# Optimization experiments

Measured on AMD Instinct MI355X. Metric: run time of the kernel, lower is better.

Reference implementation:

```python
import jax, jax.numpy as jnp
import numpy as np
from jax import lax

BATCH, FS, DIM = 32, 7, 512
E, TOPK, KD = 4, 2, 4            # experts, top-k, scan directions
N_STATE, DT_RANK = 16, 32
CAP_FACTOR, EPS, AUX_W = 1.25, 1e-6, 0.01


def _layernorm(x, g, b, eps=1e-5):
    mu = x.mean(-1, keepdims=True)
    var = ((x - mu) ** 2).mean(-1, keepdims=True)
    return (x - mu) * lax.rsqrt(var + eps) * g + b


def setup_inputs() -> dict:
    key = jax.random.key(0)
    ks = jax.random.split(key, 10)
    s = 0.02
    d = DIM
    return {
        "x": jax.random.normal(ks[0], (BATCH, FS, FS, d), jnp.float32),
        "w_gate": jax.random.normal(ks[1], (d, E)) * s,
        "b_gate": jnp.zeros((E,), jnp.float32),
        "in_proj_w": jax.random.normal(ks[2], (E, d, 2 * d)) * s,
        "in_proj_b": jnp.zeros((E, 2 * d), jnp.float32),
        "conv_w": jax.random.normal(ks[3], (E, d, 3, 3)) * s,
        "conv_b": jnp.zeros((E, d), jnp.float32),
        "x_proj_w": jax.random.normal(ks[4], (E, KD, DT_RANK + 2 * N_STATE, d)) * s,
        "dt_proj_w": jax.random.normal(ks[5], (E, KD, d, DT_RANK)) * s,
        "dt_proj_b": jax.random.normal(ks[6], (E, KD, d)) * 0.1,
        "A_log": jnp.log(jax.random.uniform(ks[7], (E, KD, d, N_STATE), minval=1.0, maxval=16.0)),
        "Ds": jnp.ones((E, KD, d), jnp.float32),
        "out_norm_g": jnp.ones((E, d), jnp.float32),
        "out_norm_b": jnp.zeros((E, d), jnp.float32),
        "norm_g": jnp.ones((E, d), jnp.float32),
        "norm_b": jnp.zeros((E, d), jnp.float32),
    }


def _ss2d_expert(x, in_w, in_b, cw, cb, xpw, dtw, dtb, A_log, Ds, og, ob, ng, nb):
    # x: [B,H,W,d]; one SS2D expert (VMamba-style, use_out_proj=False, out_norm=True)
    B, H, W, d = x.shape
    L = H * W
    xz = x @ in_w + in_b                      # [B,H,W,2d]
    xin, z = jnp.split(xz, 2, axis=-1)
    xc = jnp.transpose(xin, (0, 3, 1, 2))     # [B,d,H,W]
    xc = lax.conv_general_dilated(xc, cw[:, None, :, :], (1, 1), 'SAME',
                                  feature_group_count=d,
                                  dimension_numbers=('NCHW', 'OIHW', 'NCHW'))
    xc = jax.nn.silu(xc + cb[None, :, None, None])
    xh = xc.reshape(B, d, L)                              # row-major (h)
    xv = jnp.transpose(xc, (0, 1, 3, 2)).reshape(B, d, L)  # col-major (v)
    xs = jnp.stack([xh, xh[..., ::-1], xv, xv[..., ::-1]], axis=1)  # [B,K,d,L]

    x_dbl = jnp.einsum('bkdl,kcd->bkcl', xs, xpw)
    dt, Bm, Cm = jnp.split(x_dbl, [DT_RANK, DT_RANK + N_STATE], axis=2)
    dt = jnp.einsum('bkrl,kdr->bkdl', dt, dtw) + dtb[None, :, :, None]
    dt = jax.nn.softplus(dt)                  # [B,K,d,L]
    A = -jnp.exp(A_log)                       # [K,d,N]

    def step(h, inp):
        dt_t, B_t, C_t, x_t = inp             # [B,K,d],[B,K,N],[B,K,N],[B,K,d]
        h = h * jnp.exp(dt_t[..., None] * A) + (dt_t * x_t)[..., None] * B_t[:, :, None, :]
        y = jnp.einsum('bkdn,bkn->bkd', h, C_t)
        return h, y

    h0 = jnp.zeros((B, KD, d, N_STATE), x.dtype)
    seq = (jnp.moveaxis(dt, 3, 0), jnp.moveaxis(Bm, 3, 0),
           jnp.moveaxis(Cm, 3, 0), jnp.moveaxis(xs, 3, 0))
    _, ys = lax.scan(step, h0, seq)           # [L,B,K,d]
    ys = jnp.moveaxis(ys, 0, 3) + Ds[None, :, :, None] * xs  # [B,K,d,L]

    y = ys[:, 0] + ys[:, 1, :, ::-1]
    yv = ys[:, 2] + ys[:, 3, :, ::-1]
    y = y + jnp.transpose(yv.reshape(B, d, W, H), (0, 1, 3, 2)).reshape(B, d, L)
    y = jnp.transpose(y.reshape(B, d, H, W), (0, 2, 3, 1))   # [B,H,W,d]
    y = _layernorm(y, og, ob) * jax.nn.silu(z)
    pooled = y.mean(axis=(1, 2))              # adaptive avg pool -> [B,d]
    return _layernorm(pooled, ng, nb)


def reference(x, w_gate, b_gate, in_proj_w, in_proj_b, conv_w, conv_b, x_proj_w,
              dt_proj_w, dt_proj_b, A_log, Ds, out_norm_g, out_norm_b, norm_g, norm_b):
    B = x.shape[0]
    # gate on globally pooled features
    x_flat = x.mean(axis=(1, 2))                              # [B,dim]
    raw = jax.nn.softmax(x_flat @ w_gate + b_gate, axis=-1)   # [B,E]
    capacity = int(CAP_FACTOR * B)
    _, idx = lax.top_k(raw, TOPK)
    mask = jax.nn.one_hot(idx, E, dtype=raw.dtype).sum(axis=1)  # [B,E]
    masked = raw * mask
    denom = masked.sum(0, keepdims=True) + EPS
    gate_scores = masked / denom * capacity
    importance = raw.mean(0)
    load = mask.mean(0)
    aux_loss = AUX_W * jnp.mean((load - importance) ** 2)

    topv, topi = lax.top_k(gate_scores, TOPK)                 # [B,k]
    # dense dispatch: run every expert on the full batch (E small), then gather
    all_out = jax.vmap(_ss2d_expert, in_axes=(None,) + (0,) * 13)(
        x, in_proj_w, in_proj_b, conv_w, conv_b, x_proj_w, dt_proj_w, dt_proj_b,
        A_log, Ds, out_norm_g, out_norm_b, norm_g, norm_b)    # [E,B,dim]
    sel = all_out[topi, jnp.arange(B)[:, None]]               # [B,k,dim]
    mixed = (topv[..., None] * sel).sum(axis=1)               # [B,dim]
    return mixed, aux_loss
```

## Files before the change

kernel.cpp:

```cpp
#include <hip/hip_runtime.h>
#include <hip/hip_bf16.h>

#define B_   32
#define D_   512
#define L_   49
#define E_   4
#define KD_  4
#define NS_  16
#define RK_  32
#define JOBS_ 64

typedef short s16x8 __attribute__((ext_vector_type(8)));
typedef float f32x4v __attribute__((ext_vector_type(4)));
union U4 { uint4 u; s16x8 s; unsigned short us[8]; };

__device__ __forceinline__ float bf2f(unsigned short u){
  union{unsigned int i; float f;} v; v.i = ((unsigned int)u)<<16; return v.f;
}
__device__ __forceinline__ float2 bfp(unsigned int u){
  union{unsigned int i; float f;} a, b; a.i = u<<16; b.i = u & 0xffff0000u;
  return make_float2(a.f, b.f);
}
__device__ __forceinline__ unsigned short f2bfu(float f){
  union{float f; unsigned int i;} u; u.f = f;
  unsigned int r = u.i + 0x7fffu + ((u.i >> 16) & 1u);
  return (unsigned short)(r >> 16);
}
__device__ __forceinline__ float silu_f(float x){ return x / (1.f + expf(-x)); }

__device__ __forceinline__ float fast_exp2(float x){
  return __builtin_amdgcn_exp2f(x);
}
__device__ __forceinline__ float quad_add4(float y){
  float t1 = __uint_as_float(__builtin_amdgcn_mov_dpp(__float_as_uint(y), 0xB1, 0xF, 0xF, true));
  y += t1;
  float t2 = __uint_as_float(__builtin_amdgcn_mov_dpp(__float_as_uint(y), 0x4E, 0xF, 0xF, true));
  y += t2;
  return y;
}
__device__ __forceinline__ unsigned cvtpk_bf16(float lo, float hi){
  unsigned r; asm("v_cvt_pk_bf16_f32 %0, %1, %2" : "=v"(r) : "v"(lo), "v"(hi)); return r;
}

__device__ __forceinline__ int detect_bf(const void* x){
  unsigned short u = ((const unsigned short*)x)[threadIdx.x & 63];
  int e = (u >> 7) & 0xff;
  unsigned long long m = __ballot(e >= 96 && e < 160);
  return __popcll(m) >= 56;
}

__device__ __forceinline__ float ldf(const void* p, size_t i, int bf){
  return bf ? bf2f(((const unsigned short*)p)[i]) : ((const float*)p)[i];
}
struct f8s{ float v[8]; };
__device__ __forceinline__ f8s ldf8(const void* p, size_t i, int bf){
  f8s r;
  if (bf){
    uint4 u = *(const uint4*)((const unsigned short*)p + i);
    float2 x = bfp(u.x), y = bfp(u.y), z = bfp(u.z), w = bfp(u.w);
    r.v[0]=x.x; r.v[1]=x.y; r.v[2]=y.x; r.v[3]=y.y;
    r.v[4]=z.x; r.v[5]=z.y; r.v[6]=w.x; r.v[7]=w.y;
  } else {
    const float4* q = (const float4*)((const float*)p + i);
    float4 a = q[0], b = q[1];
    r.v[0]=a.x; r.v[1]=a.y; r.v[2]=a.z; r.v[3]=a.w;
    r.v[4]=b.x; r.v[5]=b.y; r.v[6]=b.z; r.v[7]=b.w;
  }
  return r;
}
struct f4s{ float v[4]; };
__device__ __forceinline__ f4s ldf4(const void* p, size_t i, int bf){
  f4s r;
  if (bf){
    uint2 u = *(const uint2*)((const unsigned short*)p + i);
    float2 a = bfp(u.x), b = bfp(u.y);
    r.v[0]=a.x; r.v[1]=a.y; r.v[2]=b.x; r.v[3]=b.y;
  } else {
    float4 a = *(const float4*)((const float*)p + i);
    r.v[0]=a.x; r.v[1]=a.y; r.v[2]=a.z; r.v[3]=a.w;
  }
  return r;
}
__device__ __forceinline__ U4 ldbf8(const void* p, size_t i, int bf){
  U4 r;
  if (bf){
    r.u = *(const uint4*)((const unsigned short*)p + i);
  } else {
    const float* q = (const float*)p + i;
    float4 a = *(const float4*)q, b = *(const float4*)(q+4);
    r.u.x = (unsigned)f2bfu(a.x) | ((unsigned)f2bfu(a.y) << 16);
    r.u.y = (unsigned)f2bfu(a.z) | ((unsigned)f2bfu(a.w) << 16);
    r.u.z = (unsigned)f2bfu(b.x) | ((unsigned)f2bfu(b.y) << 16);
    r.u.w = (unsigned)f2bfu(b.z) | ((unsigned)f2bfu(b.w) << 16);
  }
  return r;
}
__device__ __forceinline__ void split8(const float av[8], U4& hi, U4& lo){
  #pragma unroll
  for (int j = 0; j < 8; j++){
    union{float f; unsigned int i;} u; u.f = av[j];
    unsigned short h = (unsigned short)(u.i >> 16);
    hi.us[j] = h;
    lo.us[j] = f2bfu(av[j] - bf2f(h));
  }
}

__device__ __forceinline__ int dirmap(int k, int l){
  if (k == 0) return l;
  if (k == 1) return 48 - l;
  if (k == 2) return (l % 7) * 7 + l / 7;
  int l2 = 48 - l; return (l2 % 7) * 7 + l2 / 7;
}

__global__ __launch_bounds__(256) void k_prep(const void* __restrict__ x,
                                              const void* __restrict__ w,
                                              const void* __restrict__ wg,
                                              const void* __restrict__ bg,
                                              unsigned short* __restrict__ wt,
                                              unsigned short* __restrict__ xbf,
                                              float* __restrict__ logits){
  __shared__ unsigned short tile[64][72];
  __shared__ float red[4][4];
  __shared__ float pool[4][512];
  int bf = detect_bf(x);
  int blk = blockIdx.x;
  int t = threadIdx.x;
  if (blk < 512){
    int e = blk >> 7, cb = (blk >> 3) & 15, db = blk & 7;
    #pragma unroll
    for (int r = 0; r < 4; r++){
      int d  = r*16 + (t>>4);
      int c0 = (t&15)*4;
      size_t g = ((size_t)e*512 + db*64 + d)*1024 + cb*64 + c0;
      if (bf){
        uint2 u = *(const uint2*)((const unsigned short*)w + g);
        tile[c0+0][d] = (unsigned short)(u.x & 0xffffu);
        tile[c0+1][d] = (unsigned short)(u.x >> 16);
        tile[c0+2][d] = (unsigned short)(u.y & 0xffffu);
        tile[c0+3][d] = (unsigned short)(u.y >> 16);
      } else {
        float4 v = *(const float4*)((const float*)w + g);
        tile[c0+0][d] = f2bfu(v.x);
        tile[c0+1][d] = f2bfu(v.y);
        tile[c0+2][d] = f2bfu(v.z);
        tile[c0+3][d] = f2bfu(v.w);
      }
    }
    __syncthreads();
    #pragma unroll
    for (int r = 0; r < 2; r++){
      int o = r*256 + t;
      int c = o >> 3, d0 = (o & 7)*8;
      uint4 v = *(const uint4*)&tile[c][d0];
      *(uint4*)(wt + ((size_t)e*1024 + cb*64 + c)*512 + db*64 + d0) = v;
    }
  } else {
    int b = blk - 512;
    int wave = t >> 6, lane = t & 63;
    int d0 = lane * 8;
    float s8[8] = {};
    for (int l = wave; l < L_; l += 4){
      size_t ix = ((size_t)(b*L_ + l))*D_ + d0;
      U4 xb;
      if (bf){
        xb.u = *(const uint4*)((const unsigned short*)x + ix);
        float2 a = bfp(xb.u.x), bq = bfp(xb.u.y), c = bfp(xb.u.z), dq = bfp(xb.u.w);
        s8[0] += a.x;  s8[1] += a.y;  s8[2] += bq.x; s8[3] += bq.y;
        s8[4] += c.x;  s8[5] += c.y;  s8[6] += dq.x; s8[7] += dq.y;
      } else {
        const float* q = (const float*)x + ix;
        float4 f0 = *(const float4*)q, f1 = *(const float4*)(q+4);
        float av[8] = {f0.x,f0.y,f0.z,f0.w, f1.x,f1.y,f1.z,f1.w};
        #pragma unroll
        for (int j = 0; j < 8; j++){ xb.us[j] = f2bfu(av[j]); s8[j] += av[j]; }
      }
      *(uint4*)(xbf + ix) = xb.u;
    }
    #pragma unroll
    for (int j = 0; j < 8; j++) pool[wave][d0+j] = s8[j];
    __syncthreads();
    float p[4] = {0.f, 0.f, 0.f, 0.f};
    #pragma unroll
    for (int rep = 0; rep < 2; rep++){
      int d = t + rep*256;
      float s = pool[0][d] + pool[1][d] + pool[2][d] + pool[3][d];
      float xfd = s * (1.f/49.f);
      #pragma unroll
      for (int e = 0; e < 4; e++) p[e] = fmaf(xfd, ldf(wg, (size_t)d*E_ + e, bf), p[e]);
    }
    #pragma unroll
    for (int off = 32; off > 0; off >>= 1){
      #pragma unroll
      for (int e = 0; e < 4; e++) p[e] += __shfl_down(p[e], off, 64);
    }
    if (lane == 0){
      #pragma unroll
      for (int e = 0; e < 4; e++) red[wave][e] = p[e];
    }
    __syncthreads();
    if (t < 4)
      logits[b*4 + t] = red[0][t]+red[1][t]+red[2][t]+red[3][t] + ldf(bg, t, bf);
  }
}

__global__ __launch_bounds__(128) void k_gate2(const void* __restrict__ x,
                                               const float* __restrict__ logits,
                                               int* __restrict__ topi, float* __restrict__ topv,
                                               void* __restrict__ out){
  __shared__ float raw[B_*E_];
  __shared__ int   sel[B_];
  __shared__ float den[E_], auxp[E_];
  int bf = detect_bf(x);
  int t = threadIdx.x;
  if (t < B_){
    float l0=logits[t*4+0], l1=logits[t*4+1], l2=logits[t*4+2], l3=logits[t*4+3];
    float m = fmaxf(fmaxf(l0,l1), fmaxf(l2,l3));
    float e0=expf(l0-m), e1=expf(l1-m), e2=expf(l2-m), e3=expf(l3-m);
    float s = e0+e1+e2+e3;
    float r[4] = {e0/s, e1/s, e2/s, e3/s};
    int i1 = 0; float v1 = r[0];
    for (int e = 1; e < 4; e++) if (r[e] > v1){ v1 = r[e]; i1 = e; }
    int i2 = -1; float v2 = -1.f;
    for (int e = 0; e < 4; e++){ if (e == i1) continue; if (r[e] > v2){ v2 = r[e]; i2 = e; } }
    if (i1 < 0 || i1 > 3) i1 = 0;
    if (i2 < 0 || i2 > 3) i2 = (i1 + 1) & 3;
    sel[t] = (1<<i1) | (1<<i2);
    for (int e = 0; e < 4; e++) raw[t*4+e] = r[e];
  }
  __syncthreads();
  if (t < E_){
    float dn = 0.f, imp = 0.f, ld = 0.f;
    for (int b = 0; b < B_; b++){
      float r = raw[b*4+t];
      int bit = (sel[b] >> t) & 1;
      if (bit) dn += r;
      imp += r; ld += (float)bit;
    }
    den[t] = dn + 1e-6f;
    imp *= (1.f/B_); ld *= (1.f/B_);
    float df = ld - imp; auxp[t] = df*df;
  }
  __syncthreads();
  if (t == 0){
    float a = 0.01f * 0.25f * (auxp[0]+auxp[1]+auxp[2]+auxp[3]);
    if (bf) ((unsigned short*)out)[16384] = f2bfu(a);
    else    ((float*)out)[16384] = a;
  }
  if (t < B_){
    float gs[4];
    for (int e = 0; e < 4; e++){
      int bit = (sel[t] >> e) & 1;
      gs[e] = bit ? raw[t*4+e] * 40.f / den[e] : 0.f;
    }
    int i1 = 0; float v1 = gs[0];
    for (int e = 1; e < 4; e++) if (gs[e] > v1){ v1 = gs[e]; i1 = e; }
    int i2 = -1; float v2 = -1e30f;
    for (int e = 0; e < 4; e++){ if (e == i1) continue; if (gs[e] > v2){ v2 = gs[e]; i2 = e; } }
    if (i1 < 0 || i1 > 3) i1 = 0;
    if (i2 < 0 || i2 > 3) i2 = (i1 + 1) & 3;
    topi[t*2+0] = i1; topv[t*2+0] = v1;
    topi[t*2+1] = i2; topv[t*2+1] = v2;
  }
}

__global__ __launch_bounds__(256, 4) void k_inproj_mfma(const void* __restrict__ x,
                                                     const unsigned short* __restrict__ xbf,
                                                     const unsigned short* __restrict__ wt,
                                                     const void* __restrict__ bias,
                                                     const void* __restrict__ cw,
                                                     const void* __restrict__ cb,
                                                     const int* __restrict__ topi,
                                                     unsigned short* __restrict__ zbuf,
                                                     float* __restrict__ xc,
                                                     unsigned short* __restrict__ xchi,
                                                     unsigned short* __restrict__ xclo){
  __shared__ float xzt[49*68];
  int bf = detect_bf(x);
  int job = blockIdx.x, nt = blockIdx.y;
  int b = job >> 1;
  int e = topi[job];
  int t = threadIdx.x;
  int wave = t >> 6, lane = t & 63;
  int l16 = lane & 15, quad = lane >> 4;
  int arow = wave*16 + l16; if (arow > 48) arow = 48;
  size_t abase = ((size_t)(b*L_ + arow))*D_;
  int ct = nt*64;
  size_t bbase = ((size_t)(e*1024 + ct + l16))*D_;
  f32x4v acc[4] = {};
  #pragma unroll
  for (int k0 = 0; k0 < 512; k0 += 32){
    int k = k0 + quad*8;
    U4 a; a.u = *(const uint4*)(xbf + abase + k);
    #pragma unroll
    for (int s = 0; s < 4; s++){
      U4 bb;
      bb.u = *(const uint4*)(wt + bbase + (size_t)s*16*D_ + k);
      acc[s] = __builtin_amdgcn_mfma_f32_16x16x32_bf16(a.s, bb.s, acc[s], 0, 0, 0);
    }
  }
  int rb = wave*16 + quad*4;
  if (nt >= 8){
    #pragma unroll
    for (int s = 0; s < 4; s++){
      int c = ct + s*16 + l16;
      float bv = ldf(bias, (size_t)e*1024 + c, bf);
      #pragma unroll
      for (int r = 0; r < 4; r++){
        int row = rb + r;
        if (row < L_)
          zbuf[(size_t)job*25088 + row*D_ + (c - 512)] = f2bfu(acc[s][r] + bv);
      }
    }
    return;
  }
  #pragma unroll
  for (int s = 0; s < 4; s++){
    int cl = s*16 + l16;
    float bv = ldf(bias, (size_t)e*1024 + ct + cl, bf);
    #pragma unroll
    for (int r = 0; r < 4; r++){
      int row = rb + r;
      if (row < L_) xzt[row*68 + cl] = acc[s][r] + bv;
    }
  }
  __syncthreads();
  int c = t & 63, pg = t >> 6;
  int dch = ct + c;
  float wv[9];
  #pragma unroll
  for (int j = 0; j < 9; j++) wv[j] = ldf(cw, ((size_t)(e*D_ + dch))*9 + j, bf);
  float cbv = ldf(cb, (size_t)e*D_ + dch, bf);
  for (int p = pg; p < L_; p += 4){
    int h = p / 7, w = p % 7;
    float a2 = cbv;
    #pragma unroll
    for (int dy = 0; dy < 3; dy++){
      int hh = h + dy - 1; if (hh < 0 || hh >= 7) continue;
      #pragma unroll
      for (int dx = 0; dx < 3; dx++){
        int ww = w + dx - 1; if (ww < 0 || ww >= 7) continue;
        a2 = fmaf(xzt[(hh*7+ww)*68 + c], wv[dy*3+dx], a2);
      }
    }
    float sv = a2 * (1.f/(1.f+expf(-a2)));
    size_t oix = (size_t)job*25088 + (size_t)p*D_ + dch;
    xc[oix] = sv;
    unsigned int ui = __float_as_uint(sv);
    unsigned short hh2 = (unsigned short)(ui >> 16);
    xchi[oix] = hh2;
    xclo[oix] = f2bfu(sv - bf2f(hh2));
  }
}

__global__ __launch_bounds__(256, 4) void k_xproj(const void* __restrict__ x,
                                               const void* __restrict__ xpw,
                                               const int* __restrict__ topi,
                                               const unsigned short* __restrict__ xchi,
                                               const unsigned short* __restrict__ xclo,
                                               float* __restrict__ xdbl){
  int bf = detect_bf(x);
  int kq = blockIdx.x, job = blockIdx.y;
  int k = kq & 3, q = kq >> 2;
  int t = threadIdx.x;
  int wave = t >> 6, lane = t & 63;
  int l16 = lane & 15, quad = lane >> 4;
  int e = topi[job];
  int arow = q*16 + l16; if (arow > 48) arow = 48;
  int m = dirmap(k, arow);
  const unsigned short* ahp = xchi + (size_t)job*25088 + (size_t)m*D_;
  const unsigned short* alp = xclo + (size_t)job*25088 + (size_t)m*D_;
  size_t bbase = (((size_t)(e*KD_+k))*64 + wave*16 + l16)*D_;
  f32x4v acc = {};
  #pragma unroll
  for (int k0 = 0; k0 < 512; k0 += 32){
    int kk = k0 + quad*8;
    U4 Ahi, Alo;
    Ahi.u = *(const uint4*)(ahp + kk);
    Alo.u = *(const uint4*)(alp + kk);
    U4 bb = ldbf8(xpw, bbase + kk, bf);
    acc = __builtin_amdgcn_mfma_f32_16x16x32_bf16(Ahi.s, bb.s, acc, 0, 0, 0);
    acc = __builtin_amdgcn_mfma_f32_16x16x32_bf16(Alo.s, bb.s, acc, 0, 0, 0);
  }
  float* outb = xdbl + ((size_t)(job*KD_+k))*3136;
  int rb = q*16 + quad*4;
  int c = wave*16 + l16;
  #pragma unroll
  for (int r = 0; r < 4; r++){
    int row = rb + r;
    if (row < L_) outb[row*64 + c] = acc[r];
  }
}

__global__ __launch_bounds__(256, 2) void k_scan(const void* __restrict__ x,
                                              const void* __restrict__ dtw,
                                              const void* __restrict__ dtb_,
                                              const void* __restrict__ alog,
                                              const void* __restrict__ ds_,
                                              const int* __restrict__ topi,
                                              const float* __restrict__ xc,
                                              const float* __restrict__ xdbl,
                                              unsigned short* __restrict__ ybuf){
  int bf = detect_bf(x);
  int kz = blockIdx.x, job = blockIdx.y;
  int k = kz & 3, dz2 = kz >> 2;
  int t = threadIdx.x;
  int e = topi[job];
  int ek = e*KD_ + k;
  __shared__ float bc[49*32];
  __shared__ float dtl[49*260];
  const float* xdb = xdbl + ((size_t)(job*KD_+k))*3136;
  {
    const float4* src4 = (const float4*)xdb;
    for (int i = t; i < 392; i += 256){
      int row = i >> 3, c = i & 7;
      ((float4*)bc)[row*8 + c] = src4[row*16 + 8 + c];
    }
  }
  int w = t >> 6, lane = t & 63;
  {
    int l16 = lane & 15, quad4 = lane >> 4;
    U4 Bv[4];
    #pragma unroll
    for (int nt = 0; nt < 4; nt++){
      int d = dz2*256 + w*64 + nt*16 + l16;
      Bv[nt] = ldbf8(dtw, ((size_t)ek*D_ + d)*RK_ + quad4*8, bf);
    }
    f32x4v acc[4][4] = {};
    #pragma unroll
    for (int rt = 0; rt < 4; rt++){
      int arow = rt*16 + l16; if (arow > 48) arow = 48;
      const float* ap = xdb + arow*64 + quad4*8;
      float4 f0 = *(const float4*)ap, f1 = *(const float4*)(ap+4);
      float av[8] = {f0.x,f0.y,f0.z,f0.w, f1.x,f1.y,f1.z,f1.w};
      U4 Ahi, Alo;
      split8(av, Ahi, Alo);
      #pragma unroll
      for (int nt = 0; nt < 4; nt++){
        acc[rt][nt] = __builtin_amdgcn_mfma_f32_16x16x32_bf16(Ahi.s, Bv[nt].s, acc[rt][nt], 0, 0, 0);
        acc[rt][nt] = __builtin_amdgcn_mfma_f32_16x16x32_bf16(Alo.s, Bv[nt].s, acc[rt][nt], 0, 0, 0);
      }
    }
    #pragma unroll
    for (int nt = 0; nt < 4; nt++){
      int d = dz2*256 + w*64 + nt*16 + l16;
      float bias = ldf(dtb_, (size_t)ek*D_ + d, bf);
      int dloc = w*64 + nt*16 + l16;
      #pragma unroll
      for (int rt = 0; rt < 4; rt++){
        #pragma unroll
        for (int r = 0; r < 4; r++){
          int l = rt*16 + quad4*4 + r;
          if (l < L_){
            float v = acc[rt][nt][r] + bias;
            dtl[l*260 + dloc] = fmaxf(v, 0.f) + __logf(1.f + __expf(-fabsf(v)));
          }
        }
      }
    }
  }
  int q4 = (lane >> 2) * 4;
  int ng = lane & 3;
  int dgl = dz2*256 + w*64 + q4;
  float A2[4][4], Dsv[4];
  #pragma unroll
  for (int jj = 0; jj < 4; jj++){
    int dj = dgl + jj;
    f4s ar = ldf4(alog, ((size_t)ek*D_ + dj)*NS_ + ng*4, bf);
    #pragma unroll
    for (int n = 0; n < 4; n++) A2[jj][n] = -expf(ar.v[n]) * 1.44269504f;
    Dsv[jj] = ldf(ds_, (size_t)ek*D_ + dj, bf);
  }
  __syncthreads();
  float h[4][4];
  #pragma unroll
  for (int jj = 0; jj < 4; jj++)
    #pragma unroll
    for (int n = 0; n < 4; n++) h[jj][n] = 0.f;
  const float* xcb = xc + (size_t)job*25088;
  unsigned short* yb = ybuf + ((size_t)(job*KD_ + k))*25088;
  int dtbase = w*64 + q4;
  for (int c0 = 0; c0 < 49; c0 += 7){
    float4 xv[7];
    #pragma unroll
    for (int j = 0; j < 7; j++){
      int m = dirmap(k, c0 + j);
      xv[j] = *(const float4*)(xcb + (size_t)m*D_ + dgl);
    }
    #pragma unroll
    for (int j = 0; j < 7; j++){
      int l = c0 + j;
      float4 dt4 = *(const float4*)&dtl[l*260 + dtbase];
      float4 B4 = *(const float4*)&bc[l*32 + ng*4];
      float4 C4 = *(const float4*)&bc[l*32 + 16 + ng*4];
      float Ba[4] = {B4.x, B4.y, B4.z, B4.w};
      float Ca[4] = {C4.x, C4.y, C4.z, C4.w};
      float dta[4] = {dt4.x, dt4.y, dt4.z, dt4.w};
      float xa[4]  = {xv[j].x, xv[j].y, xv[j].z, xv[j].w};
      float ys[4];
      #pragma unroll
      for (int jj = 0; jj < 4; jj++){
        float dt = dta[jj], x_t = xa[jj];
        float dtx = dt * x_t;
        float y = 0.f;
        #pragma unroll
        for (int n = 0; n < 4; n++){
          float en = fast_exp2(dt * A2[jj][n]);
          h[jj][n] = fmaf(h[jj][n], en, dtx * Ba[n]);
          y = fmaf(h[jj][n], Ca[n], y);
        }
        y = quad_add4(y);
        ys[jj] = fmaf(Dsv[jj], x_t, y);
      }
      if (ng == 0){
        uint2 o;
        o.x = cvtpk_bf16(ys[0], ys[1]);
        o.y = cvtpk_bf16(ys[2], ys[3]);
        *(uint2*)(yb + (size_t)l*D_ + dgl) = o;
      }
    }
  }
}

__global__ __launch_bounds__(512) void k_final_a(const void* __restrict__ x,
                                                 const void* __restrict__ og,
                                                 const void* __restrict__ ob,
                                                 const int* __restrict__ topi,
                                                 const unsigned short* __restrict__ ybuf,
                                                 const unsigned short* __restrict__ zbuf,
                                                 float* __restrict__ partial){
  __shared__ float pool[8][512];
  int bf = detect_bf(x);
  int job = blockIdx.x, q = blockIdx.y, t = threadIdx.x;
  int wave = t >> 6, lane = t & 63;
  int e = topi[job];
  int d0 = lane*8;
  const unsigned short* yb = ybuf + (size_t)job*KD_*25088;
  const unsigned short* zb = zbuf + (size_t)job*25088;
  float g[8], o[8];
  {
    f8s gg = ldf8(og, (size_t)e*D_ + d0, bf);
    f8s oo = ldf8(ob, (size_t)e*D_ + d0, bf);
    #pragma unroll
    for (int j = 0; j < 8; j++){ g[j] = gg.v[j]; o[j] = oo.v[j]; }
  }
  float acc[8] = {};
  for (int i = wave; i <= 12; i += 8){
    int p = q + 4*i;
    if (p >= L_) break;
    float v[8] = {};
    #pragma unroll
    for (int k = 0; k < KD_; k++){
      int l = dirmap(k, p);
      U4 r; r.u = *(const uint4*)(yb + (size_t)k*25088 + (size_t)l*D_ + d0);
      #pragma unroll
      for (int j = 0; j < 8; j++) v[j] += bf2f(r.us[j]);
    }
    float s = 0.f, ss = 0.f;
    #pragma unroll
    for (int j = 0; j < 8; j++){ s += v[j]; ss += v[j]*v[j]; }
    #pragma unroll
    for (int off = 32; off > 0; off >>= 1){
      s  += __shfl_xor(s,  off, 64);
      ss += __shfl_xor(ss, off, 64);
    }
    float mu = s*(1.f/512.f);
    float var = ss*(1.f/512.f) - mu*mu;
    float rs = rsqrtf(var + 1e-5f);
    U4 zz; zz.u = *(const uint4*)(zb + (size_t)p*D_ + d0);
    #pragma unroll
    for (int j = 0; j < 8; j++){
      float zv = bf2f(zz.us[j]);
      acc[j] += ((v[j]-mu)*rs*g[j] + o[j]) * silu_f(zv);
    }
  }
  #pragma unroll
  for (int j = 0; j < 8; j++) pool[wave][d0+j] = acc[j];
  __syncthreads();
  float pd = pool[0][t]+pool[1][t]+pool[2][t]+pool[3][t]
           + pool[4][t]+pool[5][t]+pool[6][t]+pool[7][t];
  partial[((size_t)(job*4 + q))*512 + t] = pd;
}

__global__ __launch_bounds__(512) void k_finmix(const void* __restrict__ x,
                                                const void* __restrict__ ngg,
                                                const void* __restrict__ nbb,
                                                const int* __restrict__ topi,
                                                const float* __restrict__ topv,
                                                const float* __restrict__ partial,
                                                void* __restrict__ out){
  __shared__ float red[32];
  int bf = detect_bf(x);
  int b = blockIdx.x, t = threadIdx.x;
  int wave = t >> 6, lane = t & 63;
  int j0 = 2*b, j1 = 2*b + 1;
  int e0 = topi[j0], e1 = topi[j1];
  float g0 = topv[j0], g1 = topv[j1];
  const float* p0 = partial + (size_t)j0*4*512;
  const float* p1 = partial + (size_t)j1*4*512;
  float pd0 = (p0[t] + p0[512+t] + p0[1024+t] + p0[1536+t]) * (1.f/49.f);
  float pd1 = (p1[t] + p1[512+t] + p1[1024+t] + p1[1536+t]) * (1.f/49.f);
  float s0 = pd0, ss0 = pd0*pd0, s1 = pd1, ss1 = pd1*pd1;
  #pragma unroll
  for (int off = 32; off > 0; off >>= 1){
    s0  += __shfl_down(s0,  off, 64);
    ss0 += __shfl_down(ss0, off, 64);
    s1  += __shfl_down(s1,  off, 64);
    ss1 += __shfl_down(ss1, off, 64);
  }
  if (lane == 0){
    red[wave] = s0; red[8+wave] = ss0; red[16+wave] = s1; red[24+wave] = ss1;
  }
  __syncthreads();
  s0 = red[0]+red[1]+red[2]+red[3]+red[4]+red[5]+red[6]+red[7];
  ss0 = red[8]+red[9]+red[10]+red[11]+red[12]+red[13]+red[14]+red[15];
  s1 = red[16]+red[17]+red[18]+red[19]+red[20]+red[21]+red[22]+red[23];
  ss1 = red[24]+red[25]+red[26]+red[27]+red[28]+red[29]+red[30]+red[31];
  float mu0 = s0*(1.f/512.f), var0 = ss0*(1.f/512.f) - mu0*mu0;
  float rs0 = rsqrtf(var0 + 1e-5f);
  float mu1 = s1*(1.f/512.f), var1 = ss1*(1.f/512.f) - mu1*mu1;
  float rs1 = rsqrtf(var1 + 1e-5f);
  float v0 = ((pd0-mu0)*rs0*ldf(ngg, (size_t)e0*D_+t, bf) + ldf(nbb, (size_t)e0*D_+t, bf)) * g0;
  float v1 = ((pd1-mu1)*rs1*ldf(ngg, (size_t)e1*D_+t, bf) + ldf(nbb, (size_t)e1*D_+t, bf)) * g1;
  float v = v0 + v1;
  if (bf) ((unsigned short*)out)[b*D_ + t] = f2bfu(v);
  else    ((float*)out)[b*D_ + t] = v;
}

extern "C" void kernel_launch(void* const* d_in, const int* in_sizes, int n_in,
                              void* d_out, int out_size, void* d_ws, size_t ws_size,
                              hipStream_t stream){
  const void* x    = d_in[0];
  const void* wg   = d_in[1];
  const void* bg   = d_in[2];
  const void* ipw  = d_in[3];
  const void* ipb  = d_in[4];
  const void* cw   = d_in[5];
  const void* cb   = d_in[6];
  const void* xpw  = d_in[7];
  const void* dtw  = d_in[8];
  const void* dtb  = d_in[9];
  const void* alog = d_in[10];
  const void* dss  = d_in[11];
  const void* ogg  = d_in[12];
  const void* obb  = d_in[13];
  const void* ngg  = d_in[14];
  const void* nbb  = d_in[15];
  float* wsf = (float*)d_ws;
  int*   topi  = (int*)d_ws + 16;
  float* topv  = wsf + 96;
  float* logits= wsf + 256;
  float* xc    = wsf + 16640;
  float* xdbl  = wsf + 1622272;
  unsigned short* zbuf = (unsigned short*)(wsf + 2425088);
  unsigned short* ybuf   = (unsigned short*)(wsf + 3260672);
  unsigned short* wtrans = ybuf;
  unsigned short* xchi   = ybuf + 2097152;
  unsigned short* xclo   = ybuf + 3702784;
  unsigned short* xbf    = ybuf + 5308416;
  float* partial = wsf + 6471936;

  k_prep  <<<544, 256, 0, stream>>>(x, ipw, wg, bg, wtrans, xbf, logits);
  k_gate2 <<<1, 128, 0, stream>>>(x, logits, topi, topv, d_out);
  k_inproj_mfma<<<dim3(64,16), 256, 0, stream>>>(x, xbf, wtrans, ipb, cw, cb, topi, zbuf, xc, xchi, xclo);
  k_xproj <<<dim3(16,64), 256, 0, stream>>>(x, xpw, topi, xchi, xclo, xdbl);
  k_scan  <<<dim3(8,64), 256, 0, stream>>>(x, dtw, dtb, alog, dss, topi, xc, xdbl, ybuf);
  k_final_a<<<dim3(64,4), 512, 0, stream>>>(x, ogg, obb, topi, ybuf, zbuf, partial);
  k_finmix<<<32, 512, 0, stream>>>(x, ngg, nbb, topi, topv, partial, d_out);
}
```

Before: 218.4 us.

## Stage in-proj weight tiles through double-buffered swizzled LDS

```diff
diff --git a/kernel.cpp b/kernel.cpp
--- a/kernel.cpp
+++ b/kernel.cpp
@@ -274,7 +274,8 @@
                                                      float* __restrict__ xc,
                                                      unsigned short* __restrict__ xchi,
                                                      unsigned short* __restrict__ xclo){
-  __shared__ float xzt[49*68];
+  __shared__ unsigned short smem[2*4096];
+  float* xzt = (float*)smem;
   int bf = detect_bf(x);
   int job = blockIdx.x, nt = blockIdx.y;
   int b = job >> 1;
@@ -285,18 +286,53 @@
   int arow = wave*16 + l16; if (arow > 48) arow = 48;
   size_t abase = ((size_t)(b*L_ + arow))*D_;
   int ct = nt*64;
-  size_t bbase = ((size_t)(e*1024 + ct + l16))*D_;
+  const unsigned short* wsrc = wt + (size_t)(e*1024 + ct)*512;
   f32x4v acc[4] = {};
   #pragma unroll
-  for (int k0 = 0; k0 < 512; k0 += 32){
-    int k = k0 + quad*8;
-    U4 a; a.u = *(const uint4*)(xbf + abase + k);
-    #pragma unroll
-    for (int s = 0; s < 4; s++){
-      U4 bb;
-      bb.u = *(const uint4*)(wt + bbase + (size_t)s*16*D_ + k);
-      acc[s] = __builtin_amdgcn_mfma_f32_16x16x32_bf16(a.s, bb.s, acc[s], 0, 0, 0);
-    }
+  for (int cc = 0; cc < 2; cc++){
+    int c = t + cc*256;
+    int col = c >> 3, ko8 = c & 7;
+    uint4 v = *(const uint4*)(wsrc + (size_t)col*512 + ko8*8);
+    *(uint4*)(smem + col*64 + ((ko8 ^ (col & 7))*8)) = v;
+  }
+  U4 aA, aB;
+  aA.u = *(const uint4*)(xbf + abase + quad*8);
+  aB.u = *(const uint4*)(xbf + abase + 32 + quad*8);
+  __syncthreads();
+  for (int s = 0; s < 8; s++){
+    unsigned short* cur = smem + (s & 1)*4096;
+    U4 nA, nB;
+    if (s < 7){
+      unsigned short* nxt = smem + ((s+1) & 1)*4096;
+      int k0n = (s+1)*64;
+      #pragma unroll
+      for (int cc = 0; cc < 2; cc++){
+        int c = t + cc*256;
+        int col = c >> 3, ko8 = c & 7;
+        uint4 v = *(const uint4*)(wsrc + (size_t)col*512 + k0n + ko8*8);
+        *(uint4*)(nxt + col*64 + ((ko8 ^ (col & 7))*8)) = v;
+      }
+      nA.u = *(const uint4*)(xbf + abase + k0n + quad*8);
+      nB.u = *(const uint4*)(xbf + abase + k0n + 32 + quad*8);
+    }
+    {
+      int ko8 = quad;
+      #pragma unroll
+      for (int ss = 0; ss < 4; ss++){
+        int col = ss*16 + l16;
+        U4 bb; bb.u = *(const uint4*)(cur + col*64 + ((ko8 ^ (col & 7))*8));
+        acc[ss] = __builtin_amdgcn_mfma_f32_16x16x32_bf16(aA.s, bb.s, acc[ss], 0, 0, 0);
+      }
+      ko8 = 4 + quad;
+      #pragma unroll
+      for (int ss = 0; ss < 4; ss++){
+        int col = ss*16 + l16;
+        U4 bb; bb.u = *(const uint4*)(cur + col*64 + ((ko8 ^ (col & 7))*8));
+        acc[ss] = __builtin_amdgcn_mfma_f32_16x16x32_bf16(aB.s, bb.s, acc[ss], 0, 0, 0);
+      }
+    }
+    aA = nA; aB = nB;
+    __syncthreads();
   }
   int rb = wave*16 + quad*4;
   if (nt >= 8){
```

Measured after the change: 201.0 us. 8.0% less time.
